# Kernel optimization log

Hardware: AMD Instinct MI355X
Metric: run time of the kernel (lower is better)

Reference implementation:

```python
import jax, jax.numpy as jnp
import numpy as np

N, M, D = 2048, 2048, 16
H_INIT = 0.85


def setup_inputs() -> dict:
    key = jax.random.key(0)
    k1, k2 = jax.random.split(key)
    x = jax.random.normal(k1, (N, D), dtype=jnp.float32)
    X2 = jax.random.normal(k2, (M, D), dtype=jnp.float32)
    # log_H chosen so that softplus(log_H) == H_INIT, matching tf.Variable init
    log_H = jnp.asarray(np.log(np.exp(H_INIT) - 1.0), dtype=jnp.float32)
    return {"x": x, "X2": X2, "log_H": log_H}


def reference(x, X2, log_H):
    # fractional Brownian motion kernel:
    # K[i,j] = 0.5 * sum_d (|x_id|^2H + |X2_jd|^2H - |x_id - X2_jd|^2H)
    H = jax.nn.softplus(log_H)
    p = 2.0 * H
    # per-point terms do not depend on the other index -> sum over D first
    t1 = jnp.sum(jnp.abs(x) ** p, axis=-1)   # [N]
    t2 = jnp.sum(jnp.abs(X2) ** p, axis=-1)  # [M]
    # pairwise term: [N, M, D] broadcast, reduced over D
    t3 = jnp.sum(jnp.abs(x[:, None, :] - X2[None, :, :]) ** p, axis=-1)  # [N, M]
    K = 0.5 * (t1[:, None] + t2[None, :] - t3)
    return K
```

## Files before the change

kernel.cpp:

```cpp
#include <hip/hip_runtime.h>
#include <math.h>


#define D_DIM 16
#define BR 64
#define BC 32

typedef float v2f __attribute__((ext_vector_type(2)));

__device__ __forceinline__ float powp(float t, float p) {
    return __builtin_amdgcn_exp2f(p * __builtin_amdgcn_logf(t));
}

__global__ __launch_bounds__(256) void fbm_kernel(
    const float* __restrict__ x,
    const float* __restrict__ X2,
    const float* __restrict__ logH,
    float* __restrict__ out,
    int N, int M)
{
    __shared__ float xs[D_DIM][BR];
    __shared__ float ys[D_DIM][BC];
    __shared__ float t1s[BR];
    __shared__ float t2s[BC];

    const int tid  = threadIdx.x;
    const int brow = blockIdx.y * BR;
    const int bcol = blockIdx.x * BC;

    const float p = 2.0f * log1pf(expf(logH[0]));

    {
        float4 vx = ((const float4*)(x + (size_t)brow * D_DIM))[tid];
        int r  = tid >> 2;
        int d0 = (tid & 3) << 2;
        xs[d0 + 0][r] = vx.x; xs[d0 + 1][r] = vx.y;
        xs[d0 + 2][r] = vx.z; xs[d0 + 3][r] = vx.w;
    }
    if (tid < 128) {
        float4 vy = ((const float4*)(X2 + (size_t)bcol * D_DIM))[tid];
        int r  = tid >> 2;
        int d0 = (tid & 3) << 2;
        ys[d0 + 0][r] = vy.x; ys[d0 + 1][r] = vy.y;
        ys[d0 + 2][r] = vy.z; ys[d0 + 3][r] = vy.w;
    }
    __syncthreads();

    if (tid < BR) {
        float s = 0.0f;
        #pragma unroll
        for (int d = 0; d < D_DIM; ++d) s += powp(fabsf(xs[d][tid]), p);
        t1s[tid] = s;
    } else if (tid < BR + BC) {
        int r = tid - BR;
        float s = 0.0f;
        #pragma unroll
        for (int d = 0; d < D_DIM; ++d) s += powp(fabsf(ys[d][r]), p);
        t2s[r] = s;
    }
    __syncthreads();

    const int ti = tid >> 4;
    const int tj = tid & 15;

    const v2f pv = {p, p};
    v2f acc2[4] = {};

    #pragma unroll 4
    for (int d = 0; d < D_DIM; ++d) {
        float4 xa = *(const float4*)&xs[d][ti * 4];
        v2f bv = *(const v2f*)&ys[d][tj * 2];
        float A0 = xa.x, A1 = xa.y, A2 = xa.z, A3 = xa.w;

        #define TERM2(A_, IDX_) { \
            v2f av_; av_.x = (A_); av_.y = (A_); \
            v2f u_ = av_ - bv;                        \
            float l0_ = __builtin_amdgcn_logf(__builtin_fabsf(u_.x)); \
            float l1_ = __builtin_amdgcn_logf(__builtin_fabsf(u_.y)); \
            v2f lv_; lv_.x = l0_; lv_.y = l1_; \
            lv_ = lv_ * pv;                           \
            float e0_ = __builtin_amdgcn_exp2f(lv_.x); \
            float e1_ = __builtin_amdgcn_exp2f(lv_.y); \
            v2f ev_; ev_.x = e0_; ev_.y = e1_; \
            acc2[IDX_] += ev_;                        }

        TERM2(A0, 0)
        TERM2(A1, 1)
        TERM2(A2, 2)
        TERM2(A3, 3)
        #undef TERM2
    }

    float t2v0 = t2s[tj * 2 + 0];
    float t2v1 = t2s[tj * 2 + 1];

    #pragma unroll
    for (int a = 0; a < 4; ++a) {
        float t1v = t1s[ti * 4 + a];
        float2 o;
        o.x = 0.5f * (t1v + t2v0 - acc2[a].x);
        o.y = 0.5f * (t1v + t2v1 - acc2[a].y);
        int gi = brow + ti * 4 + a;
        *(float2*)(out + (size_t)gi * M + bcol + tj * 2) = o;
    }
}

extern "C" void kernel_launch(void* const* d_in, const int* in_sizes, int n_in,
                              void* d_out, int out_size, void* d_ws, size_t ws_size,
                              hipStream_t stream) {
    const float* x    = (const float*)d_in[0];
    const float* X2   = (const float*)d_in[1];
    const float* logH = (const float*)d_in[2];
    float* out = (float*)d_out;

    int N = in_sizes[0] / D_DIM;
    int M = in_sizes[1] / D_DIM;

    dim3 grid(M / BC, N / BR);
    dim3 block(256);
    fbm_kernel<<<grid, block, 0, stream>>>(x, X2, logH, out, N, M);
}
```

Baseline: 21.47 us.

## Replace transcendental log/exp with packed polynomial bit-trick power evaluation

Replaces the per-element hardware log2/exp2 transcendental calls with a software evaluation that works on the float's bit pattern. The exponent and mantissa are extracted, a degree-4 polynomial fitted at Chebyshev nodes approximates log2 of the mantissa, and exp2 is rebuilt from a second polynomial plus an exponent inserted by bit manipulation. The aim is to move work from the quarter-rate transcendental unit to packed FMA operations that can issue as v2f math. It adds many integer bit operations and carries approximation error, including around zero differences and with a fixed precision on the scaled exponent.

```diff
diff --git a/kernel.cpp b/kernel.cpp
--- a/kernel.cpp
+++ b/kernel.cpp
@@ -28,7 +28,62 @@
     const int brow = blockIdx.y * BR;
     const int bcol = blockIdx.x * BC;
 
-    const float p = 2.0f * log1pf(expf(logH[0]));
+    const float H = log1pf(expf(logH[0]));
+    const float p = 2.0f * H;
+
+    const float T1 = 0.475528258f, T2 = 0.293892626f;
+    const float n0 = 1.5f + T1, n1 = 1.5f + T2, n2 = 1.5f,
+                n3 = 1.5f - T2, n4 = 1.5f - T1;
+    float q4, q3, q2, q1, q0;
+    {
+        float f0 = __builtin_amdgcn_logf(n0) - (n0 - 1.0f);
+        float f1 = __builtin_amdgcn_logf(n1) - (n1 - 1.0f);
+        float f2 = __builtin_amdgcn_logf(n2) - (n2 - 1.0f);
+        float f3 = __builtin_amdgcn_logf(n3) - (n3 - 1.0f);
+        float f4 = __builtin_amdgcn_logf(n4) - (n4 - 1.0f);
+        float s1 = 0.5f * (f0 + f4), d1 = 0.5f * (f0 - f4);
+        float s2 = 0.5f * (f1 + f3), d2 = 0.5f * (f1 - f3);
+        float u1 = T1 * T1, u2 = T2 * T2;
+        float A = s1 - f2, B = s2 - f2;
+        float det = u1 * u2 * (u2 - u1);
+        float e1 = (A * u2 * u2 - B * u1 * u1) / det;
+        float e2 = (B * u1 - A * u2) / det;
+        float Ap = d1 / T1, Bp = d2 / T2;
+        float o1 = (Ap - Bp) / (u1 - u2);
+        float o0 = Ap - o1 * u1;
+        float a4 = e2;
+        float a3 = o1 - 6.0f * e2;
+        float a2 = e1 - 4.5f * o1 + 13.5f * e2;
+        float a1 = o0 - 3.0f * e1 + 6.75f * o1 - 13.5f * e2;
+        float a0 = f2 - 1.5f * o0 + 2.25f * e1 - 3.375f * o1 + 5.0625f * e2;
+        q4 = p * a4; q3 = p * a3; q2 = p * a2; q1 = p * a1;
+        q0 = p * a0 - 383.0f * p + 192.0f;
+    }
+    const float PB = p * (1.0f / 32768.0f);
+
+    float e4c, e3c, e2c, e1c, e0c;
+    {
+        float f0 = __builtin_amdgcn_exp2f(n0 - 1.0f);
+        float f1 = __builtin_amdgcn_exp2f(n1 - 1.0f);
+        float f2 = __builtin_amdgcn_exp2f(n2 - 1.0f);
+        float f3 = __builtin_amdgcn_exp2f(n3 - 1.0f);
+        float f4 = __builtin_amdgcn_exp2f(n4 - 1.0f);
+        float s1 = 0.5f * (f0 + f4), d1 = 0.5f * (f0 - f4);
+        float s2 = 0.5f * (f1 + f3), d2 = 0.5f * (f1 - f3);
+        float u1 = T1 * T1, u2 = T2 * T2;
+        float A = s1 - f2, B = s2 - f2;
+        float det = u1 * u2 * (u2 - u1);
+        float ee1 = (A * u2 * u2 - B * u1 * u1) / det;
+        float ee2 = (B * u1 - A * u2) / det;
+        float Ap = d1 / T1, Bp = d2 / T2;
+        float oo1 = (Ap - Bp) / (u1 - u2);
+        float oo0 = Ap - oo1 * u1;
+        e4c = ee2;
+        e3c = oo1 - 6.0f * ee2;
+        e2c = ee1 - 4.5f * oo1 + 13.5f * ee2;
+        e1c = oo0 - 3.0f * ee1 + 6.75f * oo1 - 13.5f * ee2;
+        e0c = f2 - 1.5f * oo0 + 2.25f * ee1 - 3.375f * oo1 + 5.0625f * ee2;
+    }
 
     {
         float4 vx = ((const float4*)(x + (size_t)brow * D_DIM))[tid];
@@ -63,7 +118,6 @@
     const int ti = tid >> 4;
     const int tj = tid & 15;
 
-    const v2f pv = {p, p};
     v2f acc2[4] = {};
 
     #pragma unroll 4
@@ -74,15 +128,37 @@
 
         #define TERM2(A_, IDX_) { \
             v2f av_; av_.x = (A_); av_.y = (A_); \
-            v2f u_ = av_ - bv;                        \
-            float l0_ = __builtin_amdgcn_logf(__builtin_fabsf(u_.x)); \
-            float l1_ = __builtin_amdgcn_logf(__builtin_fabsf(u_.y)); \
-            v2f lv_; lv_.x = l0_; lv_.y = l1_; \
-            lv_ = lv_ * pv;                           \
-            float e0_ = __builtin_amdgcn_exp2f(lv_.x); \
-            float e1_ = __builtin_amdgcn_exp2f(lv_.y); \
-            v2f ev_; ev_.x = e0_; ev_.y = e1_; \
-            acc2[IDX_] += ev_;                        }
+            v2f u_ = av_ - bv;                                    \
+            unsigned b0_ = __float_as_uint(u_.x); \
+            unsigned b1_ = __float_as_uint(u_.y); \
+            v2f hif_; \
+            hif_.x = __uint_as_float(0x4B000000u | ((b0_ >> 8) & 0x007FFFFFu)); \
+            hif_.y = __uint_as_float(0x4B000000u | ((b1_ >> 8) & 0x007FFFFFu)); \
+            v2f mm_; \
+            mm_.x = __uint_as_float((b0_ & 0x007FFFFFu) | 0x3F800000u); \
+            mm_.y = __uint_as_float((b1_ & 0x007FFFFFu) | 0x3F800000u); \
+            v2f t_ = q4; \
+            t_ = t_ * mm_ + q3; \
+            t_ = t_ * mm_ + q2; \
+            t_ = t_ * mm_ + q1; \
+            t_ = t_ * mm_ + q0; \
+            t_ = hif_ * PB + t_;                                  \
+            t_.x = fmaxf(t_.x, 128.0f); \
+            t_.y = fmaxf(t_.y, 128.0f); \
+            unsigned bt0_ = __float_as_uint(t_.x) << 7; \
+            unsigned bt1_ = __float_as_uint(t_.y) << 7; \
+            v2f sc_; \
+            sc_.x = __uint_as_float((bt0_ & 0xFF800000u) - 0x60800000u); \
+            sc_.y = __uint_as_float((bt1_ & 0xFF800000u) - 0x60800000u); \
+            v2f w_; \
+            w_.x = __uint_as_float((bt0_ & 0x007FFF80u) | 0x3F800000u); \
+            w_.y = __uint_as_float((bt1_ & 0x007FFF80u) | 0x3F800000u); \
+            v2f g_ = e4c; \
+            g_ = g_ * w_ + e3c; \
+            g_ = g_ * w_ + e2c; \
+            g_ = g_ * w_ + e1c; \
+            g_ = g_ * w_ + e0c; \
+            acc2[IDX_] += sc_ * g_; }
 
         TERM2(A0, 0)
         TERM2(A1, 1)
```

New measurement: 38.52 us. +79.4%, slower.
